# Kernel optimization log

Hardware: AMD Instinct MI355X
Metric: run time of the kernel (lower is better)

## Reference

```python
import jax, jax.numpy as jnp
import numpy as np

D_MODEL = 1024
N_HEADS = 16
HEAD = D_MODEL // N_HEADS
B, T = 4, 2048


def setup_inputs() -> dict:
    key = jax.random.key(0)
    ks = jax.random.split(key, 8)
    s = 0.02
    return {
        "x_enc": jax.random.normal(ks[0], (B, T, D_MODEL), dtype=jnp.float32),
        "x_dec": jax.random.normal(ks[1], (B, T, D_MODEL), dtype=jnp.float32),
        "mask": jnp.zeros((B, T, T), dtype=jnp.float32),
        "Wq": jax.random.normal(ks[2], (D_MODEL, D_MODEL), dtype=jnp.float32) * s,
        "bq": jnp.zeros((D_MODEL,), dtype=jnp.float32),
        "Wkv": jax.random.normal(ks[3], (D_MODEL, 2 * D_MODEL), dtype=jnp.float32) * s,
        "bkv": jnp.zeros((2 * D_MODEL,), dtype=jnp.float32),
        "Wo": jax.random.normal(ks[4], (D_MODEL, D_MODEL), dtype=jnp.float32) * s,
        "bo": jnp.zeros((D_MODEL,), dtype=jnp.float32),
    }


def reference(x_enc, x_dec, mask, Wq, bq, Wkv, bkv, Wo, bo):
    b, t, c = x_enc.shape
    # projections
    kv = x_enc @ Wkv + bkv                     # [B,T,2C]
    q = x_dec @ Wq + bq                        # [B,T,C]
    # split heads (replicates torch reshape of interleaved kv)
    kv = kv.reshape(b, t, N_HEADS, 2 * HEAD).transpose(0, 2, 1, 3)  # [B,H,T,2hs]
    q = q.reshape(b, t, N_HEADS, HEAD).transpose(0, 2, 1, 3)        # [B,H,T,hs]
    k, v = kv[..., :HEAD], kv[..., HEAD:]
    # attention
    scores = jnp.einsum("bhqd,bhkd->bhqk", q, k) / np.sqrt(HEAD).astype(np.float32)
    scores = scores + mask[:, None, :, :]      # additive mask, broadcast over heads
    attn = jax.nn.softmax(scores, axis=-1)
    res = jnp.einsum("bhqk,bhkd->bhqd", attn, v)   # [B,H,T,hs]
    res = res.transpose(0, 2, 1, 3).reshape(b, t, c)
    return res @ Wo + bo
```

## Files before the change

kernel.cpp:

```cpp
#include <hip/hip_runtime.h>
#include <hip/hip_bf16.h>
#include <math.h>


#define D_MODEL 1024
#define NH      16
#define HEAD    64
#define BATCH   4
#define SEQ     2048
#define QB      256

#define LOG2E   1.44269504088896f

typedef unsigned int   u32;
typedef unsigned short u16;
typedef __attribute__((ext_vector_type(8))) short s16x8;
typedef __attribute__((ext_vector_type(4))) float f32x4;
typedef __attribute__((ext_vector_type(4))) unsigned int u32v4;

__device__ __forceinline__ u16 tobf(float f) {
    u32 u = __builtin_bit_cast(u32, f);
    return (u16)((u + 0x7fffu + ((u >> 16) & 1u)) >> 16);
}
__device__ __forceinline__ float frombf(u16 u) {
    return __builtin_bit_cast(float, (u32)u << 16);
}
__device__ __forceinline__ u32 cvtpk(float a, float b) {
    u32 r;
    asm("v_cvt_pk_bf16_f32 %0, %1, %2" : "=v"(r) : "v"(a), "v"(b));
    return r;
}
__device__ __forceinline__ float fexp2(float x) {
    float r;
    asm("v_exp_f32 %0, %1" : "=v"(r) : "v"(x));
    return r;
}

__device__ __forceinline__ void gl_lds16(const void* g, void* l) {
    __builtin_amdgcn_global_load_lds(
        (const __attribute__((address_space(1))) u32*)g,
        (__attribute__((address_space(3))) u32*)l, 16, 0, 0);
}

__global__ __launch_bounds__(256) void prep_all(
    const float* __restrict__ x_enc, const float* __restrict__ x_dec,
    u16* __restrict__ xout, int n,
    const float* __restrict__ Wq,  u16* __restrict__ wqT,
    const float* __restrict__ Wkv, u16* __restrict__ wkvT,
    const float* __restrict__ Wo,  u16* __restrict__ woT)
{
    __shared__ __align__(16) float tile[32][33];
    const int bid = blockIdx.x;
    if (bid < 16384) {
        const int y  = bid >> 13;
        const int bx = bid & 8191;
        const float* in = y ? x_dec : x_enc;
        u16* o = xout + (size_t)y * n;
        int i = (bx * 256 + threadIdx.x) * 4;
        if (i < n) {
            float4 v = *(const float4*)(in + i);
            ushort4 ov = make_ushort4(tobf(v.x), tobf(v.y), tobf(v.z), tobf(v.w));
            *(ushort4*)(o + i) = ov;
        }
        return;
    }
    const int tb = bid - 16384;
    const int z  = tb >> 10;
    const int rb = tb & 1023;
    const int bxT = rb & 31, byT = rb >> 5;
    const int K = D_MODEL;
    const float* W = (z == 0) ? Wq : (z == 3) ? Wo : Wkv;
    u16* WT       = (z == 0) ? wqT : (z == 3) ? woT : wkvT;
    const int N   = (z == 1 || z == 2) ? 2*D_MODEL : D_MODEL;
    const int nb  = (z == 2) ? D_MODEL : 0;
    const int n0 = nb + bxT * 32, k0 = byT * 32;
    const int r = threadIdx.x >> 3, c4 = (threadIdx.x & 7) * 4;
    float4 v = *(const float4*)&W[(size_t)(k0 + r) * N + n0 + c4];
    tile[r][c4] = v.x; tile[r][c4+1] = v.y; tile[r][c4+2] = v.z; tile[r][c4+3] = v.w;
    __syncthreads();
    ushort4 o = make_ushort4(tobf(tile[c4+0][r]), tobf(tile[c4+1][r]),
                             tobf(tile[c4+2][r]), tobf(tile[c4+3][r]));
    *(ushort4*)&WT[(size_t)(n0 + r) * K + k0 + c4] = o;
}

__global__ __launch_bounds__(256) void mask_prep(
    const float* __restrict__ mask, u16* __restrict__ mp)
{
    const size_t gt = (size_t)blockIdx.x * 256 + threadIdx.x;
    const int l = (int)(gt & 63);
    const size_t tile = gt >> 6;
    const int kt = (int)(tile & 127);
    const size_t bq = tile >> 7;
    const int qt = (int)(bq & 127);
    const int b  = (int)(bq >> 7);
    const int q15 = l & 15, quad = l >> 4;
    const int q = qt*16 + q15;
    const int k = (kt >> 2)*64 + ((kt >> 1) & 1)*32 + (kt & 1)*4 + quad*8;
    float4 v = *(const float4*)&mask[((size_t)(b*SEQ + q))*SEQ + k];
    ushort4 o = make_ushort4(tobf(v.x * LOG2E), tobf(v.y * LOG2E),
                             tobf(v.z * LOG2E), tobf(v.w * LOG2E));
    *(ushort4*)&mp[tile*256 + (size_t)l*4] = o;
}

__device__ __forceinline__ void xcd_swz(int& bx, int& by) {
    const int gx = gridDim.x;
    const int nwg = gx * gridDim.y;
    const int orig = by * gx + bx;
    const int swz = (orig & 7) * (nwg >> 3) + (orig >> 3);
    bx = swz % gx; by = swz / gx;
}

__device__ __forceinline__ void store_out(u16* p, float v)  { *p = tobf(v); }
__device__ __forceinline__ void store_out(float* p, float v){ *p = v; }

template <typename OT>
__global__ __launch_bounds__(256) void gemm_bt(
    const u16* __restrict__ A, const u16* __restrict__ Bt,
    const float* __restrict__ bias, OT* __restrict__ C,
    int N, int K, float out_scale)
{
    __shared__ __align__(16) u16 As[2][128 * 32];
    __shared__ __align__(16) u16 Bs[2][128 * 32];
    const int t = threadIdx.x;
    const int w = t >> 6, l = t & 63;
    const int lane15 = l & 15, quad = l >> 4;
    int bx = blockIdx.x, by = blockIdx.y;
    xcd_swz(bx, by);
    const int m0 = by * 128, n0 = bx * 128;
    const int wm = (w >> 1) * 64, wn = (w & 1) * 64;
    const int lr = l >> 2, lk = (l & 3) * 8;

    auto stage = [&](int k0, int bufi) {
        #pragma unroll
        for (int i = 0; i < 2; ++i) {
            const int chunk = w * 2 + i;
            gl_lds16(A  + (size_t)(m0 + chunk*16 + lr) * K + k0 + lk,
                     &As[bufi][chunk * 512]);
            gl_lds16(Bt + (size_t)(n0 + chunk*16 + lr) * K + k0 + lk,
                     &Bs[bufi][chunk * 512]);
        }
    };

    f32x4 acc[4][4] = {};
    const int nb = K >> 5;
    stage(0, 0);

    for (int i = 0; i < nb; ++i) {
        const int cur = i & 1;
        __syncthreads();
        if (i + 1 < nb) stage((i + 1) << 5, cur ^ 1);
        s16x8 af[4], bfr[4];
        #pragma unroll
        for (int i2 = 0; i2 < 4; ++i2)
            af[i2] = *(const s16x8*)&As[cur][(wm + i2*16 + lane15) * 32 + quad * 8];
        #pragma unroll
        for (int j = 0; j < 4; ++j)
            bfr[j] = *(const s16x8*)&Bs[cur][(wn + j*16 + lane15) * 32 + quad * 8];
        #pragma unroll
        for (int i2 = 0; i2 < 4; ++i2)
            #pragma unroll
            for (int j = 0; j < 4; ++j)
                acc[i2][j] = __builtin_amdgcn_mfma_f32_16x16x32_bf16(
                    af[i2], bfr[j], acc[i2][j], 0, 0, 0);
    }
    #pragma unroll
    for (int j = 0; j < 4; ++j) {
        const int col = n0 + wn + j*16 + lane15;
        const float bv = bias[col];
        #pragma unroll
        for (int i = 0; i < 4; ++i)
            #pragma unroll
            for (int r = 0; r < 4; ++r) {
                const int row = m0 + wm + i*16 + quad*4 + r;
                store_out(C + (size_t)row * N + col, (acc[i][j][r] + bv) * out_scale);
            }
    }
}

__global__ __launch_bounds__(256) void gemm_kvq(
    const u16* __restrict__ xe, const u16* __restrict__ xd,
    const u16* __restrict__ wkvT, const u16* __restrict__ wqT,
    const float* __restrict__ bkv, const float* __restrict__ bq,
    u16* __restrict__ kvb, u16* __restrict__ vtb, u16* __restrict__ qbuf)
{
    const int K = D_MODEL;
    __shared__ __align__(16) u16 As[2][128 * 32];
    __shared__ __align__(16) u16 Bs[2][128 * 32];
    const int t = threadIdx.x;
    const int w = t >> 6, l = t & 63;
    const int lane15 = l & 15, quad = l >> 4;
    int bx = blockIdx.x, by = blockIdx.y;
    xcd_swz(bx, by);
    const bool isq = bx >= 16;
    const u16* A  = isq ? xd : xe;
    const u16* Bt = isq ? wqT : wkvT;
    const int n0 = (isq ? bx - 16 : bx) * 128;
    const int m0 = by * 128;
    const int wm = (w >> 1) * 64, wn = (w & 1) * 64;
    const int lr = l >> 2, lk = (l & 3) * 8;

    auto stage = [&](int k0, int bufi) {
        #pragma unroll
        for (int i = 0; i < 2; ++i) {
            const int chunk = w * 2 + i;
            gl_lds16(A  + (size_t)(m0 + chunk*16 + lr) * K + k0 + lk,
                     &As[bufi][chunk * 512]);
            gl_lds16(Bt + (size_t)(n0 + chunk*16 + lr) * K + k0 + lk,
                     &Bs[bufi][chunk * 512]);
        }
    };

    f32x4 acc[4][4] = {};
    const int nb = K >> 5;
    stage(0, 0);

    for (int i = 0; i < nb; ++i) {
        const int cur = i & 1;
        __syncthreads();
        if (i + 1 < nb) stage((i + 1) << 5, cur ^ 1);
        s16x8 af[4], bfr[4];
        #pragma unroll
        for (int i2 = 0; i2 < 4; ++i2)
            af[i2] = *(const s16x8*)&As[cur][(wm + i2*16 + lane15) * 32 + quad * 8];
        #pragma unroll
        for (int j = 0; j < 4; ++j)
            bfr[j] = *(const s16x8*)&Bs[cur][(wn + j*16 + lane15) * 32 + quad * 8];
        #pragma unroll
        for (int i2 = 0; i2 < 4; ++i2)
            #pragma unroll
            for (int j = 0; j < 4; ++j)
                acc[i2][j] = __builtin_amdgcn_mfma_f32_16x16x32_bf16(
                    af[i2], bfr[j], acc[i2][j], 0, 0, 0);
    }

    if (isq) {
        const float sc = 0.125f * LOG2E;
        #pragma unroll
        for (int j = 0; j < 4; ++j) {
            const int col = n0 + wn + j*16 + lane15;
            const float bv = bq[col];
            #pragma unroll
            for (int i = 0; i < 4; ++i)
                #pragma unroll
                for (int r = 0; r < 4; ++r) {
                    const int row = m0 + wm + i*16 + quad*4 + r;
                    qbuf[(size_t)row * D_MODEL + col] = tobf((acc[i][j][r] + bv) * sc);
                }
        }
    } else if (wn == 0) {
        #pragma unroll
        for (int j = 0; j < 4; ++j) {
            const int col = n0 + j*16 + lane15;
            const float bv = bkv[col];
            #pragma unroll
            for (int i = 0; i < 4; ++i)
                #pragma unroll
                for (int r = 0; r < 4; ++r) {
                    const int row = m0 + wm + i*16 + quad*4 + r;
                    kvb[(size_t)row * (2*D_MODEL) + col] = tobf(acc[i][j][r] + bv);
                }
        }
    } else {
        const int bh = (m0 >> 11) * NH + (n0 >> 7);
        #pragma unroll
        for (int j = 0; j < 4; ++j) {
            const int d = j*16 + lane15;
            const float bv = bkv[n0 + 64 + d];
            #pragma unroll
            for (int i = 0; i < 4; ++i) {
                const int row = m0 + wm + i*16 + quad*4;
                const int tt = row & (SEQ - 1);
                u16* p = vtb + ((size_t)bh*64 + d)*SEQ + tt;
                *(uint2*)p = make_uint2(cvtpk(acc[i][j][0]+bv, acc[i][j][1]+bv),
                                        cvtpk(acc[i][j][2]+bv, acc[i][j][3]+bv));
            }
        }
    }
}

__global__ __launch_bounds__(512, 4) void attn_mfma(
    const u16* __restrict__ qb, const u16* __restrict__ kvb,
    const u16* __restrict__ vt, const u16* __restrict__ mp,
    u16* __restrict__ resb)
{
    __shared__ __align__(16) u16 sm[4*4096];
    const int t = threadIdx.x;
    const int w = t >> 6, l = t & 63;
    const int lane15 = l & 15, quad = l >> 4;
    const int h  = blockIdx.x;
    const int q0 = blockIdx.y * QB;
    const int b  = blockIdx.z;
    const int bh = b * NH + h;
    const int lr4 = l >> 2;
    const int lc8 = (((l & 3) ^ (lr4 & 3)) * 8);
    const int cq  = (quad ^ (lane15 & 3)) * 8;
    const int kprow = (lr4 >> 2)*8 + (lr4 & 3);

    s16x8 aq0[2], aq1[2];
    #pragma unroll
    for (int s = 0; s < 2; ++s) {
        const u16* qrow = qb + (size_t)(b*SEQ + q0 + w*32 + s*16 + lane15) * D_MODEL + h*HEAD;
        aq0[s] = *(const s16x8*)(qrow + quad*8);
        aq1[s] = *(const s16x8*)(qrow + 32 + quad*8);
    }
    const u16* mrow[2];
    #pragma unroll
    for (int s = 0; s < 2; ++s)
        mrow[s] = mp + (((size_t)b*128 + (q0>>4) + w*2 + s) * 128) * 256 + (size_t)l*4;

    auto stage = [&](int k0s, int bf) {
        const int hh = w & 1, rr = w >> 1;
        const int krow = (rr >> 1)*32 + (rr & 1)*4 + kprow;
        const u16* kg = kvb + (size_t)(b*SEQ + k0s + krow) * (2*D_MODEL)
                            + h*128 + hh*32 + lc8;
        gl_lds16(kg, sm + bf*4096 + hh*2048 + rr*512);
        const u16* vg = vt + (size_t)(bh*64 + rr*16 + lr4) * SEQ
                           + k0s + hh*32 + lc8;
        gl_lds16(vg, sm + 8192 + bf*4096 + hh*2048 + rr*512);
    };

    f32x4 o_acc[2][4] = {};
    f32x4 l_acc[2] = {};
    ushort4 mreg[2][4];
    s16x8 vones;
    #pragma unroll
    for (int i = 0; i < 8; ++i) vones[i] = (short)0x3F80;

    stage(0, 0);
    #pragma unroll
    for (int s = 0; s < 2; ++s)
        #pragma unroll
        for (int nt = 0; nt < 4; ++nt)
            mreg[s][nt] = *(const ushort4*)(mrow[s] + (size_t)nt * 256);

    for (int it = 0; it < SEQ/64; ++it) {
        const int k0 = it * 64;
        const int bf = it & 1;
        __syncthreads();
        if (it + 1 < SEQ/64)
            stage(k0 + 64, bf ^ 1);

        f32x4 sv[2][4];
        #pragma unroll
        for (int s = 0; s < 2; ++s)
            #pragma unroll
            for (int nt = 0; nt < 4; ++nt) {
                sv[s][nt][0] = frombf(mreg[s][nt].x); sv[s][nt][1] = frombf(mreg[s][nt].y);
                sv[s][nt][2] = frombf(mreg[s][nt].z); sv[s][nt][3] = frombf(mreg[s][nt].w);
            }
        __builtin_amdgcn_s_setprio(1);
        #pragma unroll
        for (int nt = 0; nt < 4; ++nt) {
            s16x8 kf0 = *(const s16x8*)(sm + bf*4096 +        (nt*16 + lane15)*32 + cq);
            s16x8 kf1 = *(const s16x8*)(sm + bf*4096 + 2048 + (nt*16 + lane15)*32 + cq);
            #pragma unroll
            for (int s = 0; s < 2; ++s) {
                sv[s][nt] = __builtin_amdgcn_mfma_f32_16x16x32_bf16(kf0, aq0[s], sv[s][nt], 0, 0, 0);
                sv[s][nt] = __builtin_amdgcn_mfma_f32_16x16x32_bf16(kf1, aq1[s], sv[s][nt], 0, 0, 0);
            }
        }
        __builtin_amdgcn_s_setprio(0);

        if (it + 1 < SEQ/64) {
            #pragma unroll
            for (int s = 0; s < 2; ++s)
                #pragma unroll
                for (int nt = 0; nt < 4; ++nt)
                    mreg[s][nt] = *(const ushort4*)(mrow[s] + ((size_t)((k0+64)>>4) + nt) * 256);
        }

        s16x8 pf[2][2];
        #pragma unroll
        for (int s = 0; s < 2; ++s)
            #pragma unroll
            for (int hf = 0; hf < 2; ++hf) {
                u32v4 pk;
                pk[0] = cvtpk(fexp2(sv[s][2*hf][0]),   fexp2(sv[s][2*hf][1]));
                pk[1] = cvtpk(fexp2(sv[s][2*hf][2]),   fexp2(sv[s][2*hf][3]));
                pk[2] = cvtpk(fexp2(sv[s][2*hf+1][0]), fexp2(sv[s][2*hf+1][1]));
                pk[3] = cvtpk(fexp2(sv[s][2*hf+1][2]), fexp2(sv[s][2*hf+1][3]));
                pf[s][hf] = __builtin_bit_cast(s16x8, pk);
            }

        __builtin_amdgcn_s_setprio(1);
        #pragma unroll
        for (int s = 0; s < 2; ++s) {
            l_acc[s] = __builtin_amdgcn_mfma_f32_16x16x32_bf16(vones, pf[s][0], l_acc[s], 0, 0, 0);
            l_acc[s] = __builtin_amdgcn_mfma_f32_16x16x32_bf16(vones, pf[s][1], l_acc[s], 0, 0, 0);
        }
        #pragma unroll
        for (int dt = 0; dt < 4; ++dt) {
            s16x8 vf0 = *(const s16x8*)(sm + 8192 + bf*4096 +        (dt*16 + lane15)*32 + cq);
            s16x8 vf1 = *(const s16x8*)(sm + 8192 + bf*4096 + 2048 + (dt*16 + lane15)*32 + cq);
            #pragma unroll
            for (int s = 0; s < 2; ++s) {
                o_acc[s][dt] = __builtin_amdgcn_mfma_f32_16x16x32_bf16(vf0, pf[s][0], o_acc[s][dt], 0, 0, 0);
                o_acc[s][dt] = __builtin_amdgcn_mfma_f32_16x16x32_bf16(vf1, pf[s][1], o_acc[s][dt], 0, 0, 0);
            }
        }
        __builtin_amdgcn_s_setprio(0);
    }

    __syncthreads();
    #pragma unroll
    for (int s = 0; s < 2; ++s) {
        const float inv = 1.f / l_acc[s][0];
        u16* orow = &sm[(w*32 + s*16 + lane15) * 64];
        #pragma unroll
        for (int dt = 0; dt < 4; ++dt) {
            *(uint2*)&orow[dt*16 + quad*4] = make_uint2(
                cvtpk(o_acc[s][dt][0]*inv, o_acc[s][dt][1]*inv),
                cvtpk(o_acc[s][dt][2]*inv, o_acc[s][dt][3]*inv));
        }
    }
    __syncthreads();
    {
        const int tr = t >> 1, tc = (t & 1) * 32;
        u16* o = resb + (size_t)(b*SEQ + q0 + tr) * D_MODEL + h*HEAD + tc;
        #pragma unroll
        for (int j = 0; j < 4; ++j)
            *(uint4*)(o + j*8) = *(const uint4*)&sm[tr*64 + tc + j*8];
    }
}

extern "C" void kernel_launch(void* const* d_in, const int* in_sizes, int n_in,
                              void* d_out, int out_size, void* d_ws, size_t ws_size,
                              hipStream_t stream) {
    const float* x_enc = (const float*)d_in[0];
    const float* x_dec = (const float*)d_in[1];
    const float* mask  = (const float*)d_in[2];
    const float* Wq    = (const float*)d_in[3];
    const float* bq    = (const float*)d_in[4];
    const float* Wkv   = (const float*)d_in[5];
    const float* bkv   = (const float*)d_in[6];
    const float* Wo    = (const float*)d_in[7];
    const float* bo    = (const float*)d_in[8];
    float* out = (float*)d_out;

    const int M = BATCH * SEQ;
    u16* xe   = (u16*)d_ws;
    u16* xd   = xe   + (size_t)M * D_MODEL;
    u16* wqT  = xd   + (size_t)M * D_MODEL;
    u16* wkvT = wqT  + (size_t)D_MODEL * D_MODEL;
    u16* woT  = wkvT + (size_t)2*D_MODEL*D_MODEL;
    u16* qbuf = woT  + (size_t)D_MODEL * D_MODEL;
    u16* kvb  = qbuf + (size_t)M * D_MODEL;
    u16* vtb  = kvb  + (size_t)M * 2 * D_MODEL;
    u16* resb = vtb  + (size_t)BATCH*NH*HEAD*SEQ;
    u16* mpk  = xe;

    const int NX = M * D_MODEL;
    prep_all<<<16384 + 4096, 256, 0, stream>>>(
        x_enc, x_dec, xe, NX, Wq, wqT, Wkv, wkvT, Wo, woT);

    gemm_kvq<<<dim3(24, M/128), 256, 0, stream>>>(
        xe, xd, wkvT, wqT, bkv, bq, kvb, vtb, qbuf);
    mask_prep<<<(BATCH*128*128*64)/256, 256, 0, stream>>>(mask, mpk);
    attn_mfma<<<dim3(NH, SEQ/QB, BATCH), 512, 0, stream>>>(
        qbuf, kvb, vtb, mpk, resb);
    gemm_bt<float><<<dim3(D_MODEL/128, M/128), 256, 0, stream>>>(
        resb, woT, bo, out, D_MODEL, D_MODEL, 1.0f);
}
```

Before: 371.9 us.

## Rewrite KV/Q projection GEMM with 256x256 tiles and deep LDS pipeline

Replaces the 128x128-tile projection GEMM with a 256x256-tile, 512-thread version that uses a 128 KB LDS buffer. Loads are staged several half-tiles ahead with explicit vmcnt waits, and the LDS layout is XOR-swizzled to avoid bank conflicts. MFMA sections run at raised wave priority. The aim is more reuse per loaded byte and better overlap of global loads with MFMA work, at the cost of one block per CU and a grid of only 384 blocks, which risks tail imbalance.

```diff
diff --git a/kernel.cpp b/kernel.cpp
--- a/kernel.cpp
+++ b/kernel.cpp
@@ -177,60 +177,103 @@
     }
 }
 
-__global__ __launch_bounds__(256) void gemm_kvq(
+__global__ __launch_bounds__(512, 1) void gemm_kvq256(
     const u16* __restrict__ xe, const u16* __restrict__ xd,
     const u16* __restrict__ wkvT, const u16* __restrict__ wqT,
     const float* __restrict__ bkv, const float* __restrict__ bq,
     u16* __restrict__ kvb, u16* __restrict__ vtb, u16* __restrict__ qbuf)
 {
     const int K = D_MODEL;
-    __shared__ __align__(16) u16 As[2][128 * 32];
-    __shared__ __align__(16) u16 Bs[2][128 * 32];
+    const int NT = K / 64;
+    __shared__ __align__(16) u16 sm[65536];
+    u16* const smA = sm;
+    u16* const smB = sm + 32768;
     const int t = threadIdx.x;
     const int w = t >> 6, l = t & 63;
     const int lane15 = l & 15, quad = l >> 4;
     int bx = blockIdx.x, by = blockIdx.y;
     xcd_swz(bx, by);
-    const bool isq = bx >= 16;
+    const bool isq = bx >= 8;
     const u16* A  = isq ? xd : xe;
     const u16* Bt = isq ? wqT : wkvT;
-    const int n0 = (isq ? bx - 16 : bx) * 128;
-    const int m0 = by * 128;
-    const int wm = (w >> 1) * 64, wn = (w & 1) * 64;
-    const int lr = l >> 2, lk = (l & 3) * 8;
-
-    auto stage = [&](int k0, int bufi) {
-        #pragma unroll
-        for (int i = 0; i < 2; ++i) {
-            const int chunk = w * 2 + i;
-            gl_lds16(A  + (size_t)(m0 + chunk*16 + lr) * K + k0 + lk,
-                     &As[bufi][chunk * 512]);
-            gl_lds16(Bt + (size_t)(n0 + chunk*16 + lr) * K + k0 + lk,
-                     &Bs[bufi][chunk * 512]);
+    const int n0 = (isq ? bx - 8 : bx) * 256;
+    const int m0 = by * 256;
+    const int wm = (w >> 2) * 128;
+    const int wn = (w & 3) * 64;
+    const int lr = l >> 2;
+    const int lc8 = (((l & 3) ^ (lr & 3)) * 8);
+    const int cq  = (quad ^ (lane15 & 3)) * 8;
+
+    auto stageA = [&](int tt, int s) {
+        const int base = ((tt & 1) * 2 + s) * 256;
+        const int k0 = tt * 64 + s * 32;
+        #pragma unroll
+        for (int jj = 0; jj < 2; ++jj) {
+            const int r0 = jj * 128 + w * 16;
+            gl_lds16(A + (size_t)(m0 + r0 + lr) * K + k0 + lc8,
+                     smA + (base + r0) * 32);
         }
     };
-
-    f32x4 acc[4][4] = {};
-    const int nb = K >> 5;
-    stage(0, 0);
-
-    for (int i = 0; i < nb; ++i) {
-        const int cur = i & 1;
-        __syncthreads();
-        if (i + 1 < nb) stage((i + 1) << 5, cur ^ 1);
+    auto stageB = [&](int tt, int s) {
+        const int base = ((tt & 1) * 2 + s) * 256;
+        const int k0 = tt * 64 + s * 32;
+        #pragma unroll
+        for (int jj = 0; jj < 2; ++jj) {
+            const int r0 = jj * 128 + w * 16;
+            gl_lds16(Bt + (size_t)(n0 + r0 + lr) * K + k0 + lc8,
+                     smB + (base + r0) * 32);
+        }
+    };
+
+    f32x4 acc[8][4] = {};
+
+    stageB(0,0); stageA(0,0); stageB(0,1); stageA(0,1);
+    stageB(1,0); stageA(1,0); stageB(1,1);
+    asm volatile("s_waitcnt vmcnt(6)" ::: "memory");
+    __builtin_amdgcn_sched_barrier(0);
+    __builtin_amdgcn_s_barrier();
+
+    for (int tt = 0; tt < NT; ++tt) {
+        const int p = tt & 1;
+        const u16* Ab = smA + p * 16384;
+        const u16* Bb = smB + p * 16384;
         s16x8 af[4], bfr[4];
         #pragma unroll
-        for (int i2 = 0; i2 < 4; ++i2)
-            af[i2] = *(const s16x8*)&As[cur][(wm + i2*16 + lane15) * 32 + quad * 8];
-        #pragma unroll
-        for (int j = 0; j < 4; ++j)
-            bfr[j] = *(const s16x8*)&Bs[cur][(wn + j*16 + lane15) * 32 + quad * 8];
-        #pragma unroll
-        for (int i2 = 0; i2 < 4; ++i2)
-            #pragma unroll
-            for (int j = 0; j < 4; ++j)
-                acc[i2][j] = __builtin_amdgcn_mfma_f32_16x16x32_bf16(
-                    af[i2], bfr[j], acc[i2][j], 0, 0, 0);
+        for (int ph = 0; ph < 4; ++ph) {
+            const int s = ph >> 1;
+            const int ih = (ph & 1) * 4;
+            #pragma unroll
+            for (int i = 0; i < 4; ++i)
+                af[i] = *(const s16x8*)(Ab + s*8192 + (wm + (ih + i)*16 + lane15)*32 + cq);
+            if ((ph & 1) == 0) {
+                #pragma unroll
+                for (int j = 0; j < 4; ++j)
+                    bfr[j] = *(const s16x8*)(Bb + s*8192 + (wn + j*16 + lane15)*32 + cq);
+            }
+            if (ph == 0)      { if (tt + 1 < NT) stageA(tt + 1, 1); }
+            else if (ph == 1) { if (tt + 2 < NT) stageB(tt + 2, 0); }
+            else if (ph == 2) { if (tt + 2 < NT) stageA(tt + 2, 0); }
+            else              { if (tt + 2 < NT) stageB(tt + 2, 1); }
+            __builtin_amdgcn_sched_barrier(0);
+            __builtin_amdgcn_s_barrier();
+            asm volatile("s_waitcnt lgkmcnt(0)" ::: "memory");
+            __builtin_amdgcn_sched_barrier(0);
+            __builtin_amdgcn_s_setprio(1);
+            #pragma unroll
+            for (int i = 0; i < 4; ++i)
+                #pragma unroll
+                for (int j = 0; j < 4; ++j)
+                    acc[ih + i][j] = __builtin_amdgcn_mfma_f32_16x16x32_bf16(
+                        af[i], bfr[j], acc[ih + i][j], 0, 0, 0);
+            __builtin_amdgcn_s_setprio(0);
+            __builtin_amdgcn_sched_barrier(0);
+            if (ph == 3 && tt + 1 < NT) {
+                if (tt + 2 < NT) asm volatile("s_waitcnt vmcnt(6)" ::: "memory");
+                else             asm volatile("s_waitcnt vmcnt(0)" ::: "memory");
+                __builtin_amdgcn_sched_barrier(0);
+            }
+            __builtin_amdgcn_s_barrier();
+        }
     }
 
     if (isq) {
@@ -240,20 +283,20 @@
             const int col = n0 + wn + j*16 + lane15;
             const float bv = bq[col];
             #pragma unroll
-            for (int i = 0; i < 4; ++i)
+            for (int i = 0; i < 8; ++i)
                 #pragma unroll
                 for (int r = 0; r < 4; ++r) {
                     const int row = m0 + wm + i*16 + quad*4 + r;
                     qbuf[(size_t)row * D_MODEL + col] = tobf((acc[i][j][r] + bv) * sc);
                 }
         }
-    } else if (wn == 0) {
+    } else if ((wn & 64) == 0) {
         #pragma unroll
         for (int j = 0; j < 4; ++j) {
-            const int col = n0 + j*16 + lane15;
+            const int col = n0 + wn + j*16 + lane15;
             const float bv = bkv[col];
             #pragma unroll
-            for (int i = 0; i < 4; ++i)
+            for (int i = 0; i < 8; ++i)
                 #pragma unroll
                 for (int r = 0; r < 4; ++r) {
                     const int row = m0 + wm + i*16 + quad*4 + r;
@@ -261,18 +304,19 @@
                 }
         }
     } else {
-        const int bh = (m0 >> 11) * NH + (n0 >> 7);
+        const int head = (n0 + wn) >> 7;
+        const int bh = (m0 >> 11) * NH + head;
         #pragma unroll
         for (int j = 0; j < 4; ++j) {
             const int d = j*16 + lane15;
-            const float bv = bkv[n0 + 64 + d];
-            #pragma unroll
-            for (int i = 0; i < 4; ++i) {
+            const float bv = bkv[n0 + wn + j*16 + lane15];
+            #pragma unroll
+            for (int i = 0; i < 8; ++i) {
                 const int row = m0 + wm + i*16 + quad*4;
-                const int tt = row & (SEQ - 1);
-                u16* p = vtb + ((size_t)bh*64 + d)*SEQ + tt;
-                *(uint2*)p = make_uint2(cvtpk(acc[i][j][0]+bv, acc[i][j][1]+bv),
-                                        cvtpk(acc[i][j][2]+bv, acc[i][j][3]+bv));
+                const int tk = row & (SEQ - 1);
+                u16* pp = vtb + ((size_t)bh*64 + d)*SEQ + tk;
+                *(uint2*)pp = make_uint2(cvtpk(acc[i][j][0]+bv, acc[i][j][1]+bv),
+                                         cvtpk(acc[i][j][2]+bv, acc[i][j][3]+bv));
             }
         }
     }
@@ -453,7 +497,7 @@
     prep_all<<<16384 + 4096, 256, 0, stream>>>(
         x_enc, x_dec, xe, NX, Wq, wqT, Wkv, wkvT, Wo, woT);
 
-    gemm_kvq<<<dim3(24, M/128), 256, 0, stream>>>(
+    gemm_kvq256<<<dim3(12, 32), 512, 0, stream>>>(
         xe, xd, wkvT, wqT, bkv, bq, kvb, vtb, qbuf);
     mask_prep<<<(BATCH*128*128*64)/256, 256, 0, stream>>>(mask, mpk);
     attn_mfma<<<dim3(NH, SEQ/QB, BATCH), 512, 0, stream>>>(
```

Result: no change. 366.8 us (-1.4%).
